# Optimization experiments

Hardware: AMD Instinct MI355X
Metric: run time of the kernel (lower is better)

Reference implementation:

```python
import jax, jax.numpy as jnp
import numpy as np

N = 10000
F_IN = 512
HID = 256
N_CLS = 64


def setup_inputs() -> dict:
    key = jax.random.key(0)
    k_feat, k_adj, k_w1, k_b1, k_w2, k_b2 = jax.random.split(key, 6)
    feature = jax.random.normal(k_feat, (N, F_IN), dtype=jnp.float32)
    # normalized-adjacency-like dense matrix (sparse-ish values, scaled)
    adj = jax.random.uniform(k_adj, (N, N), dtype=jnp.float32) * (1.0 / N)
    # GCNConv params: glorot-style weights, zero bias
    s1 = 1.0 / np.sqrt(F_IN)
    s2 = 1.0 / np.sqrt(HID)
    W1 = jax.random.uniform(k_w1, (F_IN, HID), jnp.float32, -s1, s1)
    b1 = jnp.zeros((HID,), jnp.float32)
    W2 = jax.random.uniform(k_w2, (HID, N_CLS), jnp.float32, -s2, s2)
    b2 = jnp.zeros((N_CLS,), jnp.float32)
    return {"feature": feature, "adj": adj, "W1": W1, "b1": b1, "W2": W2, "b2": b2}


def gcn_conv(x, adj, W, b):
    # support = x @ W ; out = adj @ support + b
    return adj @ (x @ W) + b


def reference(feature, adj, W1, b1, W2, b2):
    x1 = jax.nn.relu(gcn_conv(feature, adj, W1, b1))
    # dropout is identity in eval mode
    x2 = gcn_conv(x1, adj, W2, b2)
    return (x1, jax.nn.log_softmax(x2, axis=1))
```

## Files before the change

kernel.cpp:

```cpp
#include <hip/hip_runtime.h>
#include <hip/hip_bf16.h>


#define NROW 10000
#define FIN  512
#define HID  256
#define NCLS 64
#define KP   10048
#define KSPLIT2 4
#define KSPAN2  2560
#define KSPLIT4 8
#define KSPAN4  1280

typedef __bf16 bf8_t __attribute__((ext_vector_type(8)));
typedef __bf16 bf4_t __attribute__((ext_vector_type(4)));
typedef float  f4_t  __attribute__((ext_vector_type(4)));

typedef __attribute__((address_space(3))) void       lds_void;
typedef const __attribute__((address_space(1))) void glb_void;

__device__ __forceinline__ void dma16(const void* g, void* l) {
    __builtin_amdgcn_global_load_lds((glb_void*)g, (lds_void*)l, 16, 0, 0);
}

__global__ void cvt_f32_bf16(const float* __restrict__ in, __bf16* __restrict__ out, int n) {
    int stride = gridDim.x * blockDim.x * 4;
    for (int i = (blockIdx.x * blockDim.x + threadIdx.x) * 4; i < n; i += stride) {
        f4_t v = *(const f4_t*)(in + i);
        bf4_t o;
        o[0] = (__bf16)v[0]; o[1] = (__bf16)v[1]; o[2] = (__bf16)v[2]; o[3] = (__bf16)v[3];
        *(bf4_t*)(out + i) = o;
    }
}

__global__ void cvt_transpose(const float* __restrict__ in, __bf16* __restrict__ out, int K, int Nn) {
    int idx = blockIdx.x * 256 + threadIdx.x;
    if (idx < K * Nn) {
        int k = idx / Nn, n = idx % Nn;
        out[n * K + k] = (__bf16)in[idx];
    }
}

template<int BN, bool AF32, int EPI>
__global__ void __launch_bounds__(256, (BN >= 256) ? 3 : 4)
gemm_bt(const void* __restrict__ Ap, const __bf16* __restrict__ Bt,
        int M, int Nn, int K, int Kclamp, int lda, int ldb, int kspan,
        float* __restrict__ outF, __bf16* __restrict__ outB,
        int ldo, long partStride)
{
    constexpr int BM = 64, BK = 64;
    constexpr int WM = BM / 2, WN = BN / 2;
    constexpr int MI = WM / 16, NI = WN / 16;
    constexpr int BCALLS = BN / 32;
    constexpr int ACALLS = BM / 32;
    __shared__ __bf16 As[BM * BK];
    __shared__ __bf16 Bs[BN * BK];

    const int tid  = threadIdx.x;
    const int lane = tid & 63;
    const int wave = tid >> 6;
    const int wm = wave >> 1, wn = wave & 1;
    const int m0 = blockIdx.x * BM;
    const int n0 = blockIdx.y * BN;
    const int kbase = blockIdx.z * kspan;
    const int kend  = min(K, kbase + kspan);

    f4_t acc[MI][NI];
    #pragma unroll
    for (int i = 0; i < MI; i++)
        #pragma unroll
        for (int j = 0; j < NI; j++)
            acc[i][j] = f4_t{0.f, 0.f, 0.f, 0.f};

    const int lrow  = lane & 15;
    const int koff0 = (lane >> 4) * 8;

    const __bf16* Brow[BCALLS];
    #pragma unroll
    for (int j = 0; j < BCALLS; ++j) {
        int c = wave + j * 4;
        Brow[j] = Bt + (long)(n0 + c * 8 + (lane >> 3)) * ldb + (lane & 7) * 8;
    }
    const float* Arow[4];
    int Acol[4], AldsOff[4];
    const __bf16* ArowB[ACALLS];
    if constexpr (AF32) {
        #pragma unroll
        for (int i = 0; i < 4; ++i) {
            int idx = tid + i * 256;
            int r = idx >> 4, c4 = idx & 15;
            Arow[i] = (const float*)Ap + (long)min(m0 + r, M - 1) * lda;
            Acol[i] = c4 * 4;
            AldsOff[i] = r * BK + c4 * 4;
        }
    } else {
        #pragma unroll
        for (int j = 0; j < ACALLS; ++j) {
            int c = wave + j * 4;
            ArowB[j] = (const __bf16*)Ap + (long)(m0 + c * 8 + (lane >> 3)) * lda + (lane & 7) * 8;
        }
    }

    for (int k0 = kbase; k0 < kend; k0 += BK) {
        if constexpr (AF32) {
            f4_t av[4];
            #pragma unroll
            for (int i = 0; i < 4; ++i)
                av[i] = *(const f4_t*)(Arow[i] + min(k0 + Acol[i], Kclamp - 4));
            #pragma unroll
            for (int i = 0; i < 4; ++i) {
                bf4_t o;
                o[0] = (__bf16)av[i][0]; o[1] = (__bf16)av[i][1];
                o[2] = (__bf16)av[i][2]; o[3] = (__bf16)av[i][3];
                *(bf4_t*)&As[AldsOff[i]] = o;
            }
        } else {
            #pragma unroll
            for (int j = 0; j < ACALLS; ++j)
                dma16(ArowB[j] + k0, &As[(wave + j * 4) * 512]);
        }
        #pragma unroll
        for (int j = 0; j < BCALLS; ++j)
            dma16(Brow[j] + k0, &Bs[(wave + j * 4) * 512]);

        __syncthreads();

        #pragma unroll
        for (int ks = 0; ks < BK; ks += 32) {
            bf8_t af[MI], bfv[NI];
            #pragma unroll
            for (int mi = 0; mi < MI; mi++)
                af[mi] = *(const bf8_t*)&As[(wm * WM + mi * 16 + lrow) * BK + ks + koff0];
            #pragma unroll
            for (int ni = 0; ni < NI; ni++)
                bfv[ni] = *(const bf8_t*)&Bs[(wn * WN + ni * 16 + lrow) * BK + ks + koff0];
            #pragma unroll
            for (int mi = 0; mi < MI; mi++)
                #pragma unroll
                for (int ni = 0; ni < NI; ni++)
                    acc[mi][ni] = __builtin_amdgcn_mfma_f32_16x16x32_bf16(
                        af[mi], bfv[ni], acc[mi][ni], 0, 0, 0);
        }
        __syncthreads();
    }

    const int erow = wm * WM + (lane >> 4) * 4;
    const int ecol = wn * WN + lrow;
    #pragma unroll
    for (int mi = 0; mi < MI; mi++) {
        #pragma unroll
        for (int ni = 0; ni < NI; ni++) {
            #pragma unroll
            for (int r = 0; r < 4; r++) {
                int grow = m0 + erow + mi * 16 + r;
                int gcol = n0 + ecol + ni * 16;
                if (grow < M && gcol < Nn) {
                    float v = acc[mi][ni][r];
                    if constexpr (EPI == 0) {
                        outB[(long)grow * ldo + gcol] = (__bf16)v;
                    } else {
                        outF[blockIdx.z * partStride + (long)grow * ldo + gcol] = v;
                    }
                }
            }
        }
    }
}

__global__ void relu_bias_fin(const float* __restrict__ part, const float* __restrict__ b1,
                              float* __restrict__ outF, __bf16* __restrict__ outB) {
    long i = (long)(blockIdx.x * 256 + threadIdx.x) * 4;
    f4_t v = *(const f4_t*)(part + i);
    #pragma unroll
    for (int s = 1; s < KSPLIT2; s++) {
        f4_t p = *(const f4_t*)(part + (long)s * NROW * HID + i);
        v[0] += p[0]; v[1] += p[1]; v[2] += p[2]; v[3] += p[3];
    }
    int col = (int)(i & (HID - 1));
    f4_t b = *(const f4_t*)(b1 + col);
    f4_t y;
    bf4_t yb;
    #pragma unroll
    for (int j = 0; j < 4; j++) {
        y[j] = fmaxf(v[j] + b[j], 0.f);
        yb[j] = (__bf16)y[j];
    }
    *(f4_t*)(outF + i) = y;
    *(bf4_t*)(outB + i) = yb;
}

__global__ void logsoftmax_fin(const float* __restrict__ part, const float* __restrict__ b2,
                               float* __restrict__ out, int M) {
    int row  = blockIdx.x * 4 + (threadIdx.x >> 6);
    int lane = threadIdx.x & 63;
    if (row >= M) return;
    float v = b2[lane];
    #pragma unroll
    for (int s = 0; s < KSPLIT4; s++) v += part[((long)s * M + row) * NCLS + lane];
    float m = v;
    #pragma unroll
    for (int off = 32; off > 0; off >>= 1) m = fmaxf(m, __shfl_xor(m, off));
    float e = __expf(v - m);
    float sum = e;
    #pragma unroll
    for (int off = 32; off > 0; off >>= 1) sum += __shfl_xor(sum, off);
    out[(long)row * NCLS + lane] = (v - m) - __logf(sum);
}

extern "C" void kernel_launch(void* const* d_in, const int* in_sizes, int n_in,
                              void* d_out, int out_size, void* d_ws, size_t ws_size,
                              hipStream_t stream) {
    const float* feat = (const float*)d_in[0];
    const float* adj  = (const float*)d_in[1];
    const float* W1   = (const float*)d_in[2];
    const float* b1   = (const float*)d_in[3];
    const float* W2   = (const float*)d_in[4];
    const float* b2   = (const float*)d_in[5];
    float* out = (float*)d_out;
    char* ws = (char*)d_ws;

    __bf16* featb = (__bf16*)(ws);
    __bf16* W1t   = (__bf16*)(ws + 10289152);
    __bf16* W2t   = (__bf16*)(ws + 10551296);
    __bf16* S1t   = (__bf16*)(ws + 10584064);
    __bf16* x1b   = (__bf16*)(ws + 15728640);
    __bf16* S2t   = (__bf16*)(ws + 20873216);
    float*  part  = (float*) (ws + 22159360);

    hipMemsetAsync(S1t, 0, (size_t)HID * KP * 2, stream);
    hipMemsetAsync(S2t, 0, (size_t)NCLS * KP * 2, stream);

    cvt_f32_bf16<<<640, 256, 0, stream>>>(feat, featb, NROW * FIN);
    cvt_transpose<<<(FIN * HID + 255) / 256, 256, 0, stream>>>(W1, W1t, FIN, HID);
    cvt_transpose<<<(HID * NCLS + 255) / 256, 256, 0, stream>>>(W2, W2t, HID, NCLS);

    gemm_bt<64, false, 0><<<dim3(4, 157, 1), 256, 0, stream>>>(
        W1t, featb, HID, NROW, FIN, FIN, FIN, FIN, FIN,
        nullptr, S1t, KP, 0);

    gemm_bt<256, true, 2><<<dim3(157, 1, KSPLIT2), 256, 0, stream>>>(
        adj, S1t, NROW, HID, KP, NROW, NROW, KP, KSPAN2,
        part, nullptr, HID, (long)NROW * HID);

    relu_bias_fin<<<NROW * HID / 4 / 256, 256, 0, stream>>>(part, b1, out, x1b);

    gemm_bt<64, false, 0><<<dim3(1, 157, 1), 256, 0, stream>>>(
        W2t, x1b, NCLS, NROW, HID, HID, HID, HID, HID,
        nullptr, S2t, KP, 0);

    gemm_bt<64, true, 2><<<dim3(157, 1, KSPLIT4), 256, 0, stream>>>(
        adj, S2t, NROW, NCLS, KP, NROW, NROW, KP, KSPAN4,
        part, nullptr, NCLS, (long)NROW * NCLS);

    logsoftmax_fin<<<2500, 256, 0, stream>>>(part, b2, out + (long)NROW * HID, NROW);
}
```

Measured before the change: 738.0 us.

## Pre-convert adjacency to padded bf16 once and feed GEMMs via LDS DMA

```diff
diff --git a/kernel.cpp b/kernel.cpp
--- a/kernel.cpp
+++ b/kernel.cpp
@@ -33,6 +33,25 @@
     }
 }
 
+__global__ void cvt_adj_bf16(const float* __restrict__ adj, __bf16* __restrict__ adjb) {
+    const int r = blockIdx.x;
+    const float* src = adj + (long)r * NROW;
+    __bf16* dst = adjb + (long)r * KP;
+    for (int ch = threadIdx.x; ch < KP / 8; ch += 256) {
+        bf8_t o;
+        if (r < NROW && ch < NROW / 8) {
+            f4_t a = *(const f4_t*)(src + ch * 8);
+            f4_t b = *(const f4_t*)(src + ch * 8 + 4);
+            o[0] = (__bf16)a[0]; o[1] = (__bf16)a[1]; o[2] = (__bf16)a[2]; o[3] = (__bf16)a[3];
+            o[4] = (__bf16)b[0]; o[5] = (__bf16)b[1]; o[6] = (__bf16)b[2]; o[7] = (__bf16)b[3];
+        } else {
+            o = bf8_t{(__bf16)0.f, (__bf16)0.f, (__bf16)0.f, (__bf16)0.f,
+                      (__bf16)0.f, (__bf16)0.f, (__bf16)0.f, (__bf16)0.f};
+        }
+        *(bf8_t*)(dst + ch * 8) = o;
+    }
+}
+
 __global__ void cvt_transpose(const float* __restrict__ in, __bf16* __restrict__ out, int K, int Nn) {
     int idx = blockIdx.x * 256 + threadIdx.x;
     if (idx < K * Nn) {
@@ -41,10 +60,10 @@
     }
 }
 
-template<int BN, bool AF32, int EPI>
+template<int BN, int EPI>
 __global__ void __launch_bounds__(256, (BN >= 256) ? 3 : 4)
-gemm_bt(const void* __restrict__ Ap, const __bf16* __restrict__ Bt,
-        int M, int Nn, int K, int Kclamp, int lda, int ldb, int kspan,
+gemm_bt(const __bf16* __restrict__ Ab, const __bf16* __restrict__ Bt,
+        int M, int Nn, int K, int lda, int ldb, int kspan,
         float* __restrict__ outF, __bf16* __restrict__ outB,
         int ldo, long partStride)
 {
@@ -81,44 +100,17 @@
         int c = wave + j * 4;
         Brow[j] = Bt + (long)(n0 + c * 8 + (lane >> 3)) * ldb + (lane & 7) * 8;
     }
-    const float* Arow[4];
-    int Acol[4], AldsOff[4];
-    const __bf16* ArowB[ACALLS];
-    if constexpr (AF32) {
-        #pragma unroll
-        for (int i = 0; i < 4; ++i) {
-            int idx = tid + i * 256;
-            int r = idx >> 4, c4 = idx & 15;
-            Arow[i] = (const float*)Ap + (long)min(m0 + r, M - 1) * lda;
-            Acol[i] = c4 * 4;
-            AldsOff[i] = r * BK + c4 * 4;
-        }
-    } else {
-        #pragma unroll
-        for (int j = 0; j < ACALLS; ++j) {
-            int c = wave + j * 4;
-            ArowB[j] = (const __bf16*)Ap + (long)(m0 + c * 8 + (lane >> 3)) * lda + (lane & 7) * 8;
-        }
+    const __bf16* Arow[ACALLS];
+    #pragma unroll
+    for (int j = 0; j < ACALLS; ++j) {
+        int c = wave + j * 4;
+        Arow[j] = Ab + (long)(m0 + c * 8 + (lane >> 3)) * lda + (lane & 7) * 8;
     }
 
     for (int k0 = kbase; k0 < kend; k0 += BK) {
-        if constexpr (AF32) {
-            f4_t av[4];
-            #pragma unroll
-            for (int i = 0; i < 4; ++i)
-                av[i] = *(const f4_t*)(Arow[i] + min(k0 + Acol[i], Kclamp - 4));
-            #pragma unroll
-            for (int i = 0; i < 4; ++i) {
-                bf4_t o;
-                o[0] = (__bf16)av[i][0]; o[1] = (__bf16)av[i][1];
-                o[2] = (__bf16)av[i][2]; o[3] = (__bf16)av[i][3];
-                *(bf4_t*)&As[AldsOff[i]] = o;
-            }
-        } else {
-            #pragma unroll
-            for (int j = 0; j < ACALLS; ++j)
-                dma16(ArowB[j] + k0, &As[(wave + j * 4) * 512]);
-        }
+        #pragma unroll
+        for (int j = 0; j < ACALLS; ++j)
+            dma16(Arow[j] + k0, &As[(wave + j * 4) * 512]);
         #pragma unroll
         for (int j = 0; j < BCALLS; ++j)
             dma16(Brow[j] + k0, &Bs[(wave + j * 4) * 512]);
@@ -226,30 +218,32 @@
     __bf16* x1b   = (__bf16*)(ws + 15728640);
     __bf16* S2t   = (__bf16*)(ws + 20873216);
     float*  part  = (float*) (ws + 22159360);
+    __bf16* adjb  = (__bf16*)(ws + 63119360);
 
     hipMemsetAsync(S1t, 0, (size_t)HID * KP * 2, stream);
     hipMemsetAsync(S2t, 0, (size_t)NCLS * KP * 2, stream);
 
     cvt_f32_bf16<<<640, 256, 0, stream>>>(feat, featb, NROW * FIN);
+    cvt_adj_bf16<<<KP, 256, 0, stream>>>(adj, adjb);
     cvt_transpose<<<(FIN * HID + 255) / 256, 256, 0, stream>>>(W1, W1t, FIN, HID);
     cvt_transpose<<<(HID * NCLS + 255) / 256, 256, 0, stream>>>(W2, W2t, HID, NCLS);
 
-    gemm_bt<64, false, 0><<<dim3(4, 157, 1), 256, 0, stream>>>(
-        W1t, featb, HID, NROW, FIN, FIN, FIN, FIN, FIN,
+    gemm_bt<64, 0><<<dim3(4, 157, 1), 256, 0, stream>>>(
+        W1t, featb, HID, NROW, FIN, FIN, FIN, FIN,
         nullptr, S1t, KP, 0);
 
-    gemm_bt<256, true, 2><<<dim3(157, 1, KSPLIT2), 256, 0, stream>>>(
-        adj, S1t, NROW, HID, KP, NROW, NROW, KP, KSPAN2,
+    gemm_bt<256, 2><<<dim3(157, 1, KSPLIT2), 256, 0, stream>>>(
+        adjb, S1t, NROW, HID, KP, KP, KP, KSPAN2,
         part, nullptr, HID, (long)NROW * HID);
 
     relu_bias_fin<<<NROW * HID / 4 / 256, 256, 0, stream>>>(part, b1, out, x1b);
 
-    gemm_bt<64, false, 0><<<dim3(1, 157, 1), 256, 0, stream>>>(
-        W2t, x1b, NCLS, NROW, HID, HID, HID, HID, HID,
+    gemm_bt<64, 0><<<dim3(1, 157, 1), 256, 0, stream>>>(
+        W2t, x1b, NCLS, NROW, HID, HID, HID, HID,
         nullptr, S2t, KP, 0);
 
-    gemm_bt<64, true, 2><<<dim3(157, 1, KSPLIT4), 256, 0, stream>>>(
-        adj, S2t, NROW, NCLS, KP, NROW, NROW, KP, KSPAN4,
+    gemm_bt<64, 2><<<dim3(157, 1, KSPLIT4), 256, 0, stream>>>(
+        adjb, S2t, NROW, NCLS, KP, KP, KP, KSPAN4,
         part, nullptr, NCLS, (long)NROW * NCLS);
 
     logsoftmax_fin<<<2500, 256, 0, stream>>>(part, b2, out + (long)NROW * HID, NROW);
```

Measured after the change: 760.5 us. +3.0%, slower.

## Double-buffer LDS tiles, XOR-swizzle bf16 layouts, and split big GEMM into 128-wide N tiles

Applied to the files above, without the earlier changes.

```diff
diff --git a/kernel.cpp b/kernel.cpp
--- a/kernel.cpp
+++ b/kernel.cpp
@@ -23,13 +23,19 @@
     __builtin_amdgcn_global_load_lds((glb_void*)g, (lds_void*)l, 16, 0, 0);
 }
 
-__global__ void cvt_f32_bf16(const float* __restrict__ in, __bf16* __restrict__ out, int n) {
+__device__ __forceinline__ int swzc(int k, int r) {
+    return (k & ~63) | ((((k >> 3) & 7) ^ (r & 7)) << 3) | (k & 7);
+}
+
+template<int LDW>
+__global__ void cvt_f32_bf16_swz(const float* __restrict__ in, __bf16* __restrict__ out, int n) {
     int stride = gridDim.x * blockDim.x * 4;
     for (int i = (blockIdx.x * blockDim.x + threadIdx.x) * 4; i < n; i += stride) {
         f4_t v = *(const f4_t*)(in + i);
         bf4_t o;
         o[0] = (__bf16)v[0]; o[1] = (__bf16)v[1]; o[2] = (__bf16)v[2]; o[3] = (__bf16)v[3];
-        *(bf4_t*)(out + i) = o;
+        int row = i / LDW, k = i & (LDW - 1);
+        *(bf4_t*)(out + (long)row * LDW + swzc(k, row)) = o;
     }
 }
 
@@ -37,12 +43,12 @@
     int idx = blockIdx.x * 256 + threadIdx.x;
     if (idx < K * Nn) {
         int k = idx / Nn, n = idx % Nn;
-        out[n * K + k] = (__bf16)in[idx];
+        out[(long)n * K + swzc(k, n)] = (__bf16)in[idx];
     }
 }
 
 template<int BN, bool AF32, int EPI>
-__global__ void __launch_bounds__(256, (BN >= 256) ? 3 : 4)
+__global__ void __launch_bounds__(256, (BN >= 128) ? 3 : 4)
 gemm_bt(const void* __restrict__ Ap, const __bf16* __restrict__ Bt,
         int M, int Nn, int K, int Kclamp, int lda, int ldb, int kspan,
         float* __restrict__ outF, __bf16* __restrict__ outB,
@@ -51,10 +57,11 @@
     constexpr int BM = 64, BK = 64;
     constexpr int WM = BM / 2, WN = BN / 2;
     constexpr int MI = WM / 16, NI = WN / 16;
+    constexpr int ACALLS = BM / 32;
     constexpr int BCALLS = BN / 32;
-    constexpr int ACALLS = BM / 32;
-    __shared__ __bf16 As[BM * BK];
-    __shared__ __bf16 Bs[BN * BK];
+    constexpr int ASZ = BM * BK, BSZ = BN * BK;
+    __shared__ __bf16 As[2 * ASZ];
+    __shared__ __bf16 Bs[2 * BSZ];
 
     const int tid  = threadIdx.x;
     const int lane = tid & 63;
@@ -74,6 +81,7 @@
 
     const int lrow  = lane & 15;
     const int koff0 = (lane >> 4) * 8;
+    const int l7    = lrow & 7;
 
     const __bf16* Brow[BCALLS];
     #pragma unroll
@@ -81,17 +89,17 @@
         int c = wave + j * 4;
         Brow[j] = Bt + (long)(n0 + c * 8 + (lane >> 3)) * ldb + (lane & 7) * 8;
     }
-    const float* Arow[4];
+    const __bf16* ArowB[ACALLS];
+    const float*  ArowF[4];
     int Acol[4], AldsOff[4];
-    const __bf16* ArowB[ACALLS];
     if constexpr (AF32) {
         #pragma unroll
         for (int i = 0; i < 4; ++i) {
             int idx = tid + i * 256;
             int r = idx >> 4, c4 = idx & 15;
-            Arow[i] = (const float*)Ap + (long)min(m0 + r, M - 1) * lda;
+            ArowF[i] = (const float*)Ap + (long)min(m0 + r, M - 1) * lda;
             Acol[i] = c4 * 4;
-            AldsOff[i] = r * BK + c4 * 4;
+            AldsOff[i] = r * BK + ((((c4 >> 1) ^ (r & 7)) << 3) | ((c4 & 1) * 4));
         }
     } else {
         #pragma unroll
@@ -101,39 +109,59 @@
         }
     }
 
+    if constexpr (AF32) {
+        f4_t av[4];
+        #pragma unroll
+        for (int i = 0; i < 4; ++i)
+            av[i] = *(const f4_t*)(ArowF[i] + min(kbase + Acol[i], Kclamp - 4));
+        #pragma unroll
+        for (int i = 0; i < 4; ++i) {
+            bf4_t o;
+            o[0] = (__bf16)av[i][0]; o[1] = (__bf16)av[i][1];
+            o[2] = (__bf16)av[i][2]; o[3] = (__bf16)av[i][3];
+            *(bf4_t*)&As[AldsOff[i]] = o;
+        }
+    } else {
+        #pragma unroll
+        for (int j = 0; j < ACALLS; ++j)
+            dma16(ArowB[j] + kbase, &As[(wave + j * 4) * 512]);
+    }
+    #pragma unroll
+    for (int j = 0; j < BCALLS; ++j)
+        dma16(Brow[j] + kbase, &Bs[(wave + j * 4) * 512]);
+    __syncthreads();
+
+    int cur = 0;
     for (int k0 = kbase; k0 < kend; k0 += BK) {
-        if constexpr (AF32) {
-            f4_t av[4];
-            #pragma unroll
-            for (int i = 0; i < 4; ++i)
-                av[i] = *(const f4_t*)(Arow[i] + min(k0 + Acol[i], Kclamp - 4));
-            #pragma unroll
-            for (int i = 0; i < 4; ++i) {
-                bf4_t o;
-                o[0] = (__bf16)av[i][0]; o[1] = (__bf16)av[i][1];
-                o[2] = (__bf16)av[i][2]; o[3] = (__bf16)av[i][3];
-                *(bf4_t*)&As[AldsOff[i]] = o;
+        const bool has_next = (k0 + BK < kend);
+        const int nxt = cur ^ 1;
+        f4_t av[4];
+        if (has_next) {
+            if constexpr (AF32) {
+                #pragma unroll
+                for (int i = 0; i < 4; ++i)
+                    av[i] = *(const f4_t*)(ArowF[i] + min(k0 + BK + Acol[i], Kclamp - 4));
+            } else {
+                #pragma unroll
+                for (int j = 0; j < ACALLS; ++j)
+                    dma16(ArowB[j] + (k0 + BK), &As[nxt * ASZ + (wave + j * 4) * 512]);
             }
-        } else {
-            #pragma unroll
-            for (int j = 0; j < ACALLS; ++j)
-                dma16(ArowB[j] + k0, &As[(wave + j * 4) * 512]);
-        }
-        #pragma unroll
-        for (int j = 0; j < BCALLS; ++j)
-            dma16(Brow[j] + k0, &Bs[(wave + j * 4) * 512]);
-
-        __syncthreads();
+            #pragma unroll
+            for (int j = 0; j < BCALLS; ++j)
+                dma16(Brow[j] + (k0 + BK), &Bs[nxt * BSZ + (wave + j * 4) * 512]);
+        }
 
         #pragma unroll
         for (int ks = 0; ks < BK; ks += 32) {
+            const int cc = (ks + koff0) >> 3;
+            const int co = ((cc ^ l7) << 3);
             bf8_t af[MI], bfv[NI];
             #pragma unroll
             for (int mi = 0; mi < MI; mi++)
-                af[mi] = *(const bf8_t*)&As[(wm * WM + mi * 16 + lrow) * BK + ks + koff0];
+                af[mi] = *(const bf8_t*)&As[cur * ASZ + (wm * WM + mi * 16 + lrow) * BK + co];
             #pragma unroll
             for (int ni = 0; ni < NI; ni++)
-                bfv[ni] = *(const bf8_t*)&Bs[(wn * WN + ni * 16 + lrow) * BK + ks + koff0];
+                bfv[ni] = *(const bf8_t*)&Bs[cur * BSZ + (wn * WN + ni * 16 + lrow) * BK + co];
             #pragma unroll
             for (int mi = 0; mi < MI; mi++)
                 #pragma unroll
@@ -141,7 +169,20 @@
                     acc[mi][ni] = __builtin_amdgcn_mfma_f32_16x16x32_bf16(
                         af[mi], bfv[ni], acc[mi][ni], 0, 0, 0);
         }
+
+        if (has_next) {
+            if constexpr (AF32) {
+                #pragma unroll
+                for (int i = 0; i < 4; ++i) {
+                    bf4_t o;
+                    o[0] = (__bf16)av[i][0]; o[1] = (__bf16)av[i][1];
+                    o[2] = (__bf16)av[i][2]; o[3] = (__bf16)av[i][3];
+                    *(bf4_t*)&As[nxt * ASZ + AldsOff[i]] = o;
+                }
+            }
+        }
         __syncthreads();
+        cur ^= 1;
     }
 
     const int erow = wm * WM + (lane >> 4) * 4;
@@ -157,7 +198,7 @@
                 if (grow < M && gcol < Nn) {
                     float v = acc[mi][ni][r];
                     if constexpr (EPI == 0) {
-                        outB[(long)grow * ldo + gcol] = (__bf16)v;
+                        outB[(long)grow * ldo + swzc(gcol, grow)] = (__bf16)v;
                     } else {
                         outF[blockIdx.z * partStride + (long)grow * ldo + gcol] = v;
                     }
@@ -176,6 +217,7 @@
         f4_t p = *(const f4_t*)(part + (long)s * NROW * HID + i);
         v[0] += p[0]; v[1] += p[1]; v[2] += p[2]; v[3] += p[3];
     }
+    int row = (int)(i >> 8);
     int col = (int)(i & (HID - 1));
     f4_t b = *(const f4_t*)(b1 + col);
     f4_t y;
@@ -186,7 +228,7 @@
         yb[j] = (__bf16)y[j];
     }
     *(f4_t*)(outF + i) = y;
-    *(bf4_t*)(outB + i) = yb;
+    *(bf4_t*)(outB + (long)row * HID + swzc(col, row)) = yb;
 }
 
 __global__ void logsoftmax_fin(const float* __restrict__ part, const float* __restrict__ b2,
@@ -230,7 +272,7 @@
     hipMemsetAsync(S1t, 0, (size_t)HID * KP * 2, stream);
     hipMemsetAsync(S2t, 0, (size_t)NCLS * KP * 2, stream);
 
-    cvt_f32_bf16<<<640, 256, 0, stream>>>(feat, featb, NROW * FIN);
+    cvt_f32_bf16_swz<FIN><<<640, 256, 0, stream>>>(feat, featb, NROW * FIN);
     cvt_transpose<<<(FIN * HID + 255) / 256, 256, 0, stream>>>(W1, W1t, FIN, HID);
     cvt_transpose<<<(HID * NCLS + 255) / 256, 256, 0, stream>>>(W2, W2t, HID, NCLS);
 
@@ -238,7 +280,7 @@
         W1t, featb, HID, NROW, FIN, FIN, FIN, FIN, FIN,
         nullptr, S1t, KP, 0);
 
-    gemm_bt<256, true, 2><<<dim3(157, 1, KSPLIT2), 256, 0, stream>>>(
+    gemm_bt<128, true, 2><<<dim3(157, 2, KSPLIT2), 256, 0, stream>>>(
         adj, S1t, NROW, HID, KP, NROW, NROW, KP, KSPAN2,
         part, nullptr, HID, (long)NROW * HID);
 
```

Result: no change. 737.5 us (-0.1%).
